# Kernel tuning notes

Measured on AMD Instinct MI355X. Metric: run time of the kernel, lower is better.

The kernel has to match this reference:

```python
import jax, jax.numpy as jnp
import numpy as np

# Architecture dims (from setArch args)
B, IN = 256, 1024          # batch, inputSize
E, H1, S = 32, 1024, 512   # numStateEnsembles, stateHiddenLayerSize, stateEnsembleOutputSize
H2, F = 512, 64            # featureHiddenLayerSize, numStateFeatures
NO, HO, OF = 16, 512, 1    # numOutputEnsembles, outputEnsembleHiddenLayerSize, outputEnsembleFeatures
T = E * F                  # thalamusSpaceSize
TIN = IN + T               # totalInputSize


def setup_inputs() -> dict:
    key = jax.random.key(0)
    ks = jax.random.split(key, 14)
    sc = 0.02
    f32 = jnp.float32
    return {
        "inputs": jax.random.normal(ks[0], (B, IN), f32),
        # stacked state-ensemble params: Linear(TIN,H1) -> Softplus -> Linear(H1,S)
        "sw1": jax.random.normal(ks[1], (E, TIN, H1), f32) * sc,
        "sb1": jax.random.normal(ks[2], (E, H1), f32) * sc,
        "sw2": jax.random.normal(ks[3], (E, H1, S), f32) * sc,
        "sb2": jax.random.normal(ks[4], (E, S), f32) * sc,
        # stacked feature-ensemble params: Linear(S,H2) -> ReLU -> Linear(H2,F)
        "fw1": jax.random.normal(ks[5], (E, S, H2), f32) * sc,
        "fb1": jax.random.normal(ks[6], (E, H2), f32) * sc,
        "fw2": jax.random.normal(ks[7], (E, H2, F), f32) * sc,
        "fb2": jax.random.normal(ks[8], (E, F), f32) * sc,
        # stacked output-ensemble params: Linear(S+1,HO) -> ReLU -> Linear(HO,OF)
        "ow1": jax.random.normal(ks[9], (NO, S + 1, HO), f32) * sc,
        "ob1": jax.random.normal(ks[10], (NO, HO), f32) * sc,
        "ow2": jax.random.normal(ks[11], (NO, HO, OF), f32) * sc,
        "ob2": jax.random.normal(ks[12], (NO, OF), f32) * sc,
        "action": 1,
        "context": 3,
        "num_iterations": 4,
    }


def reference(inputs, sw1, sb1, sw2, sb2, fw1, fb1, fw2, fb2,
              ow1, ob1, ow2, ob2, action, context, num_iterations):
    b = inputs.shape[0]
    # resetThalamus: savedThalamusFeatures = zeros(E*F)
    thal = jnp.zeros((b, T), inputs.dtype)
    state = None
    for _ in range(num_iterations):
        # leInput = cat(thalamusFeatures, inputs)  -> [B, TIN]
        x = jnp.concatenate([thal, inputs], axis=-1)
        # all E state ensembles batched: Linear -> Softplus -> Linear
        h = jax.nn.softplus(jnp.einsum('bi,eih->beh', x, sw1) + sb1)   # [B,E,H1]
        state = jnp.einsum('beh,ehs->bes', h, sw2) + sb2               # [B,E,S]
        # all E feature ensembles batched: Linear -> ReLU -> Linear
        g = jax.nn.relu(jnp.einsum('bes,esh->beh', state, fw1) + fb1)  # [B,E,H2]
        feat = jnp.einsum('beh,ehf->bef', g, fw2) + fb2                # [B,E,F]
        # thalamusFeatures = concatenate(computedFeatures)
        thal = feat.reshape(b, T)
    # output ensemble for `context` on cat([action], stateValues[context])
    sc_state = state[:, context, :]                                    # [B,S]
    a = jnp.full((b, 1), action, inputs.dtype)
    y = jnp.concatenate([a, sc_state], axis=-1)                        # [B,S+1]
    z = jax.nn.relu(y @ ow1[context] + ob1[context])                   # [B,HO]
    reward = z @ ow2[context] + ob2[context]                           # [B,OF]
    return reward
```

## Files before the change

### kernel.cpp

```cpp
#include <hip/hip_runtime.h>
#include <hip/hip_bf16.h>

#define B_SZ 256
#define IN_  1024
#define E_   32
#define H1_  1024
#define S_   512
#define H2_  512
#define F_   64
#define T_   2048
#define TIN_ 3072
#define NO_  16
#define HO_  512

typedef __attribute__((ext_vector_type(8))) short bf16x8;
typedef __attribute__((ext_vector_type(4))) float f32x4;

__device__ __forceinline__ unsigned short f2bf(float f) {
    unsigned u = __builtin_bit_cast(unsigned, f);
    u += 0x7fffu + ((u >> 16) & 1u);
    return (unsigned short)(u >> 16);
}
__device__ __forceinline__ float bf2f(unsigned short h) {
    return __builtin_bit_cast(float, ((unsigned)h) << 16);
}
__device__ __forceinline__ float softplusf(float x) {
    return fmaxf(x, 0.0f) + log1pf(expf(-fabsf(x)));
}
__device__ __forceinline__ void gload_lds16(const void* g, void* l) {
    __builtin_amdgcn_global_load_lds(
        (const __attribute__((address_space(1))) unsigned int*)g,
        (__attribute__((address_space(3))) unsigned int*)l,
        16, 0, 0);
}

__global__ __launch_bounds__(256) void cvt_t64(const float* __restrict__ in,
                                               unsigned short* __restrict__ out,
                                               int K, int N) {
    __shared__ float tile[64][65];
    const size_t eoff = (size_t)blockIdx.z * K * N;
    const float* ip = in + eoff;
    unsigned short* op = out + eoff;
    const int k0 = blockIdx.x * 64, n0 = blockIdx.y * 64;
    const int t = threadIdx.x;
    const int lr = t >> 4;
    const int lc = (t & 15) << 2;
    #pragma unroll
    for (int i = 0; i < 4; ++i) {
        const float4 v = *(const float4*)&ip[(size_t)(k0 + lr + 16 * i) * N + n0 + lc];
        float* dst = &tile[lr + 16 * i][lc];
        dst[0] = v.x; dst[1] = v.y; dst[2] = v.z; dst[3] = v.w;
    }
    __syncthreads();
    #pragma unroll
    for (int i = 0; i < 4; ++i) {
        const int n = (t >> 4) + 16 * i;
        const int k = (t & 15) << 2;
        ushort4 o;
        o.x = f2bf(tile[k][n]); o.y = f2bf(tile[k + 1][n]);
        o.z = f2bf(tile[k + 2][n]); o.w = f2bf(tile[k + 3][n]);
        *(ushort4*)&op[(size_t)(n0 + n) * K + k0 + k] = o;
    }
}

__global__ void x_init(const float* __restrict__ inp, unsigned short* __restrict__ x) {
    const int i = blockIdx.x * 256 + threadIdx.x;
    const int b = i / (IN_ / 4), c = (i % (IN_ / 4)) * 4;
    const float4 v = *(const float4*)&inp[(size_t)b * IN_ + c];
    ushort4 o;
    o.x = f2bf(v.x); o.y = f2bf(v.y); o.z = f2bf(v.z); o.w = f2bf(v.w);
    *(ushort4*)&x[(size_t)b * TIN_ + T_ + c] = o;
}

template<int BM, int BN, int TPB, int ACT, int ADD_BASE, int OUTM>
__global__ __launch_bounds__(TPB) void gemm_k(
    const unsigned short* __restrict__ A, int lda, long strideAe,
    int kOff, int K,
    const unsigned short* __restrict__ W, int ldw, long strideWe,
    const float* __restrict__ bias,
    const float* __restrict__ baseBuf,
    void* __restrict__ out, void* __restrict__ out2,
    int ldc, long strideOe, int N)
{
    constexpr int NW = TPB / 64;
    constexpr int WM_ = 2, WN_ = NW / 2;
    constexpr int MI = BM / (16 * WM_), NI = BN / (16 * WN_);
    constexpr int AL = (BM * 4) / TPB, BL = (BN * 4) / TPB;
    __shared__ unsigned short As0[BM * 32], Bs0[BN * 32];
    __shared__ unsigned short As1[BM * 32], Bs1[BN * 32];
    const int e = blockIdx.z;
    const int m0 = blockIdx.x * BM;
    const int n0 = blockIdx.y * BN;
    const int tid = threadIdx.x;
    const int wid = tid >> 6;
    const int lane = tid & 63;
    const int wm = wid / WN_, wn = wid % WN_;
    const unsigned short* Ae = A + (size_t)e * strideAe + (size_t)m0 * lda + kOff;
    const unsigned short* We = W + (size_t)e * strideWe + (size_t)n0 * ldw + kOff;

    f32x4 acc[MI][NI];
    #pragma unroll
    for (int i = 0; i < MI; ++i)
        #pragma unroll
        for (int j = 0; j < NI; ++j) {
            f32x4 z = {0.f, 0.f, 0.f, 0.f};
            acc[i][j] = z;
        }

    const int lr = lane & 15;
    const int lk = (lane >> 4) << 3;

    auto stage = [&](unsigned short* Asb, unsigned short* Bsb, int kt) {
        const int kk = kt * 32;
        #pragma unroll
        for (int p = 0; p < AL; ++p) {
            const int seg = p * TPB + tid;
            const int r = seg >> 2, c = (seg & 3) << 3;
            gload_lds16(Ae + (size_t)r * lda + kk + c, Asb + ((size_t)(p * TPB + wid * 64)) * 8);
        }
        #pragma unroll
        for (int p = 0; p < BL; ++p) {
            const int seg = p * TPB + tid;
            const int r = seg >> 2, c = (seg & 3) << 3;
            gload_lds16(We + (size_t)r * ldw + kk + c, Bsb + ((size_t)(p * TPB + wid * 64)) * 8);
        }
    };
    auto compute = [&](const unsigned short* Asb, const unsigned short* Bsb) {
        bf16x8 af[MI], bfv[NI];
        #pragma unroll
        for (int mi = 0; mi < MI; ++mi)
            af[mi] = *(const bf16x8*)&Asb[(wm * MI * 16 + mi * 16 + lr) * 32 + lk];
        #pragma unroll
        for (int ni = 0; ni < NI; ++ni)
            bfv[ni] = *(const bf16x8*)&Bsb[(wn * NI * 16 + ni * 16 + lr) * 32 + lk];
        #pragma unroll
        for (int mi = 0; mi < MI; ++mi)
            #pragma unroll
            for (int ni = 0; ni < NI; ++ni)
                acc[mi][ni] = __builtin_amdgcn_mfma_f32_16x16x32_bf16(
                    af[mi], bfv[ni], acc[mi][ni], 0, 0, 0);
    };

    const int nt = K / 32;
    stage(As0, Bs0, 0);
    __syncthreads();
    for (int t = 0; t < nt; t += 2) {
        stage(As1, Bs1, t + 1);
        compute(As0, Bs0);
        __syncthreads();
        if (t + 2 < nt) stage(As0, Bs0, t + 2);
        compute(As1, Bs1);
        __syncthreads();
    }

    const int lg = lane >> 4;
    #pragma unroll
    for (int ni = 0; ni < NI; ++ni) {
        const int col = n0 + wn * NI * 16 + ni * 16 + lr;
        const float bv = bias ? bias[(size_t)e * N + col] : 0.0f;
        #pragma unroll
        for (int mi = 0; mi < MI; ++mi) {
            #pragma unroll
            for (int r = 0; r < 4; ++r) {
                const int row = m0 + wm * MI * 16 + mi * 16 + lg * 4 + r;
                float v = acc[mi][ni][r] + bv;
                if constexpr (ADD_BASE) v += baseBuf[((size_t)e * B_SZ + row) * H1_ + col];
                if constexpr (ACT == 1) v = softplusf(v);
                if constexpr (ACT == 2) v = fmaxf(v, 0.0f);
                const size_t oidx = (size_t)e * strideOe + (size_t)row * ldc + col;
                if constexpr (OUTM == 2) {
                    ((float*)out)[oidx] = v;
                    ((unsigned short*)out2)[oidx] = f2bf(softplusf(v));
                } else {
                    ((unsigned short*)out)[oidx] = f2bf(v);
                }
            }
        }
    }
}

__global__ __launch_bounds__(512) void head_z(const unsigned short* __restrict__ state,
                                              const float* __restrict__ ow1,
                                              const float* __restrict__ ob1,
                                              const int* __restrict__ actp,
                                              const int* __restrict__ ctxp,
                                              float* __restrict__ z) {
    __shared__ float ys[16][516];
    const int ctx = *ctxp;
    const float act = (float)(*actp);
    const int b0 = blockIdx.x * 16;
    const int t = threadIdx.x;
    for (int bb = 0; bb < 16; ++bb)
        ys[bb][1 + t] = bf2f(state[((size_t)(ctx * B_SZ + b0 + bb)) * S_ + t]);
    if (t < 16) ys[t][0] = act;
    __syncthreads();
    const float* w = ow1 + (size_t)ctx * (S_ + 1) * HO_;
    float acc[16];
    #pragma unroll
    for (int bb = 0; bb < 16; ++bb) acc[bb] = 0.0f;
    for (int k = 0; k < S_ + 1; ++k) {
        const float wv = w[(size_t)k * HO_ + t];
        #pragma unroll
        for (int bb = 0; bb < 16; ++bb) acc[bb] += ys[bb][k] * wv;
    }
    const float b1 = ob1[ctx * HO_ + t];
    for (int bb = 0; bb < 16; ++bb)
        z[(size_t)(b0 + bb) * HO_ + t] = fmaxf(acc[bb] + b1, 0.0f);
}

__global__ void head_r(const float* __restrict__ z, const float* __restrict__ ow2,
                       const float* __restrict__ ob2, const int* __restrict__ ctxp,
                       float* __restrict__ out) {
    const int ctx = *ctxp;
    const int b = blockIdx.x;
    const int t = threadIdx.x;
    const float* w = ow2 + (size_t)ctx * HO_;
    float s = 0.0f;
    for (int h = t; h < HO_; h += 64) s += z[(size_t)b * HO_ + h] * w[h];
    #pragma unroll
    for (int off = 32; off; off >>= 1) s += __shfl_down(s, off);
    if (t == 0) out[b] = s + ob2[ctx];
}

extern "C" void kernel_launch(void* const* d_in, const int* in_sizes, int n_in,
                              void* d_out, int out_size, void* d_ws, size_t ws_size,
                              hipStream_t stream) {
    (void)in_sizes; (void)n_in; (void)out_size; (void)ws_size;
    const float* inputs = (const float*)d_in[0];
    const float* sw1 = (const float*)d_in[1];
    const float* sb1 = (const float*)d_in[2];
    const float* sw2 = (const float*)d_in[3];
    const float* sb2 = (const float*)d_in[4];
    const float* fw1 = (const float*)d_in[5];
    const float* fb1 = (const float*)d_in[6];
    const float* fw2 = (const float*)d_in[7];
    const float* fb2 = (const float*)d_in[8];
    const float* ow1 = (const float*)d_in[9];
    const float* ob1 = (const float*)d_in[10];
    const float* ow2 = (const float*)d_in[11];
    const float* ob2 = (const float*)d_in[12];
    const int* actp = (const int*)d_in[13];
    const int* ctxp = (const int*)d_in[14];

    char* p = (char*)d_ws;
    unsigned short* w1t = (unsigned short*)p; p += (size_t)E_ * H1_ * TIN_ * 2;
    unsigned short* w2t = (unsigned short*)p; p += (size_t)E_ * S_ * H1_ * 2;
    unsigned short* f1t = (unsigned short*)p; p += (size_t)E_ * H2_ * S_ * 2;
    unsigned short* f2t = (unsigned short*)p; p += (size_t)E_ * F_ * H2_ * 2;
    unsigned short* xbf = (unsigned short*)p; p += (size_t)B_SZ * TIN_ * 2;
    float* base = (float*)p;                  p += (size_t)E_ * B_SZ * H1_ * 4;
    unsigned short* hbf = (unsigned short*)p; p += (size_t)E_ * B_SZ * H1_ * 2;
    unsigned short* stbf = (unsigned short*)p; p += (size_t)E_ * B_SZ * S_ * 2;
    unsigned short* gbf = (unsigned short*)p; p += (size_t)E_ * B_SZ * H2_ * 2;
    float* zbuf = (float*)p;                  p += (size_t)B_SZ * HO_ * 4;

    cvt_t64<<<dim3(TIN_ / 64, H1_ / 64, E_), 256, 0, stream>>>(sw1, w1t, TIN_, H1_);
    cvt_t64<<<dim3(H1_ / 64, S_ / 64, E_),  256, 0, stream>>>(sw2, w2t, H1_, S_);
    cvt_t64<<<dim3(S_ / 64, H2_ / 64, E_),  256, 0, stream>>>(fw1, f1t, S_, H2_);
    cvt_t64<<<dim3(H2_ / 64, F_ / 64, E_),  256, 0, stream>>>(fw2, f2t, H2_, F_);
    x_init<<<(B_SZ * IN_ / 4) / 256, 256, 0, stream>>>(inputs, xbf);

    gemm_k<128, 128, 512, 0, 0, 2><<<dim3(2, H1_ / 128, E_), 512, 0, stream>>>(
        xbf, TIN_, 0L, T_, IN_, w1t, TIN_, (long)H1_ * TIN_, sb1, nullptr,
        base, hbf, H1_, (long)B_SZ * H1_, H1_);

    for (int it = 0; it < 4; ++it) {
        if (it > 0) {
            gemm_k<128, 128, 512, 1, 1, 0><<<dim3(2, H1_ / 128, E_), 512, 0, stream>>>(
                xbf, TIN_, 0L, 0, T_, w1t, TIN_, (long)H1_ * TIN_, nullptr, base,
                hbf, nullptr, H1_, (long)B_SZ * H1_, H1_);
        }
        gemm_k<64, 64, 256, 0, 0, 0><<<dim3(4, S_ / 64, E_), 256, 0, stream>>>(
            hbf, H1_, (long)B_SZ * H1_, 0, H1_, w2t, H1_, (long)S_ * H1_, sb2, nullptr,
            stbf, nullptr, S_, (long)B_SZ * S_, S_);
        if (it < 3) {
            gemm_k<64, 64, 256, 2, 0, 0><<<dim3(4, H2_ / 64, E_), 256, 0, stream>>>(
                stbf, S_, (long)B_SZ * S_, 0, S_, f1t, S_, (long)H2_ * S_, fb1, nullptr,
                gbf, nullptr, H2_, (long)B_SZ * H2_, H2_);
            gemm_k<64, 64, 256, 0, 0, 0><<<dim3(4, 1, E_), 256, 0, stream>>>(
                gbf, H2_, (long)B_SZ * H2_, 0, H2_, f2t, H2_, (long)F_ * H2_, fb2, nullptr,
                xbf, nullptr, TIN_, 64L, F_);
        }
    }
    head_z<<<B_SZ / 16, 512, 0, stream>>>(stbf, ow1, ob1, actp, ctxp, zbuf);
    head_r<<<B_SZ, 64, 0, stream>>>(zbuf, ow2, ob2, ctxp, (float*)d_out);
}
```

Before: 804.2 us.

## Add swizzled 64-wide-K GEMM kernel with interleaved MFMA/LDS scheduling for main layers

```diff
diff --git a/kernel.cpp b/kernel.cpp
--- a/kernel.cpp
+++ b/kernel.cpp
@@ -70,6 +70,171 @@
     ushort4 o;
     o.x = f2bf(v.x); o.y = f2bf(v.y); o.z = f2bf(v.z); o.w = f2bf(v.w);
     *(ushort4*)&x[(size_t)b * TIN_ + T_ + c] = o;
+}
+
+#define RD_A(RHALF, PTR)                                                          \
+    _Pragma("unroll") for (int i_ = 0; i_ < 2; ++i_)                              \
+    _Pragma("unroll") for (int kh_ = 0; kh_ < 2; ++kh_) {                         \
+        const int mi_ = (RHALF) * 2 + i_;                                         \
+        const int row_ = wm * 64 + mi_ * 16 + lr;                                 \
+        af[mi_][kh_] = *(const bf16x8*)((PTR) + row_ * 64 +                       \
+                       ((((kh_ << 2) + lg) ^ (row_ & 7)) << 3));                  \
+    }
+#define RD_B(NHALF, PTR)                                                          \
+    _Pragma("unroll") for (int j_ = 0; j_ < 2; ++j_)                              \
+    _Pragma("unroll") for (int kh_ = 0; kh_ < 2; ++kh_) {                         \
+        const int ni_ = (NHALF) * 2 + j_;                                         \
+        const int row_ = wn * 64 + ni_ * 16 + lr;                                 \
+        bfr[ni_][kh_] = *(const bf16x8*)((PTR) + row_ * 64 +                      \
+                        ((((kh_ << 2) + lg) ^ (row_ & 7)) << 3));                 \
+    }
+#define MMQ(RH, NH)                                                               \
+    _Pragma("unroll") for (int i_ = 0; i_ < 2; ++i_)                              \
+    _Pragma("unroll") for (int j_ = 0; j_ < 2; ++j_)                              \
+    _Pragma("unroll") for (int kh_ = 0; kh_ < 2; ++kh_)                           \
+        acc[(RH)*2+i_][(NH)*2+j_] = __builtin_amdgcn_mfma_f32_16x16x32_bf16(      \
+            af[(RH)*2+i_][kh_], bfr[(NH)*2+j_][kh_], acc[(RH)*2+i_][(NH)*2+j_],   \
+            0, 0, 0);
+
+template<int TPB, int ACT, int ADD_BASE, int OUTM>
+__global__ __launch_bounds__(TPB, 2) void gemm8(
+    const unsigned short* __restrict__ A, int lda, long strideAe,
+    int kOff, int K,
+    const unsigned short* __restrict__ W, int ldw, long strideWe,
+    const float* __restrict__ bias,
+    const float* __restrict__ baseBuf,
+    void* __restrict__ out, void* __restrict__ out2,
+    int ldc, long strideOe, int N)
+{
+    constexpr int BM = 128;
+    constexpr int NW = TPB / 64;
+    constexpr int WN_ = NW / 2;
+    constexpr int BN = 64 * WN_;
+    constexpr int RA = (64 * 8) / TPB;
+    constexpr int RB = ((BN / 2) * 8) / TPB;
+    constexpr int LQ = 2 * (RA + RB);
+
+    __shared__ unsigned short As[2][BM * 64];
+    __shared__ unsigned short Bs[2][BN * 64];
+
+    const int NB = N / BN;
+    const int bid = blockIdx.x;
+    const int pairs = gridDim.x >> 1;
+    const int mhalf = (bid >= pairs) ? 1 : 0;
+    const int pr = bid - mhalf * pairs;
+    const int n0 = (pr % NB) * BN;
+    const int e  = pr / NB;
+    const int m0 = mhalf * BM;
+
+    const int tid = threadIdx.x;
+    const int wid = tid >> 6;
+    const int lane = tid & 63;
+    const int wm = wid / WN_, wn = wid % WN_;
+    const int lr = lane & 15;
+    const int lg = lane >> 4;
+
+    const unsigned short* Ae = A + (size_t)e * strideAe + (size_t)m0 * lda + kOff;
+    const unsigned short* We = W + (size_t)e * strideWe + (size_t)n0 * ldw + kOff;
+
+    f32x4 acc[4][4];
+    #pragma unroll
+    for (int i = 0; i < 4; ++i)
+        #pragma unroll
+        for (int j = 0; j < 4; ++j) {
+            f32x4 z = {0.f, 0.f, 0.f, 0.f};
+            acc[i][j] = z;
+        }
+    bf16x8 af[4][2], bfr[4][2];
+
+    auto issueGroup = [&](int kt, int bufI) {
+        const int kk = kt << 6;
+        unsigned short* Ad = &As[bufI][0];
+        unsigned short* Bd = &Bs[bufI][0];
+        #pragma unroll
+        for (int h = 0; h < 2; ++h)
+            #pragma unroll
+            for (int rr = 0; rr < RA; ++rr) {
+                const int seg = rr * TPB + tid;
+                const int row = h * 64 + (seg >> 3);
+                gload_lds16(Ae + (size_t)row * lda + kk + (((seg & 7) ^ (row & 7)) << 3),
+                            Ad + (size_t)(h * 64 * 64) + (size_t)(rr * TPB + (wid << 6)) * 8);
+            }
+        #pragma unroll
+        for (int h = 0; h < 2; ++h)
+            #pragma unroll
+            for (int rr = 0; rr < RB; ++rr) {
+                const int seg = rr * TPB + tid;
+                const int row = h * (BN / 2) + (seg >> 3);
+                gload_lds16(We + (size_t)row * ldw + kk + (((seg & 7) ^ (row & 7)) << 3),
+                            Bd + (size_t)(h * (BN / 2) * 64) + (size_t)(rr * TPB + (wid << 6)) * 8);
+            }
+    };
+
+    const int nt = K >> 6;
+    issueGroup(0, 0);
+    if (nt > 1) issueGroup(1, 1);
+
+    for (int t = 0; t < nt; ++t) {
+        const int c = t & 1;
+        const unsigned short* Ab = &As[c][0];
+        const unsigned short* Bb = &Bs[c][0];
+        if (t + 1 < nt) { asm volatile("s_waitcnt vmcnt(%0)" :: "i"(LQ) : "memory"); }
+        else            { asm volatile("s_waitcnt vmcnt(0)" ::: "memory"); }
+        __builtin_amdgcn_sched_barrier(0);
+        __builtin_amdgcn_s_barrier();
+        RD_A(0, Ab); RD_B(0, Bb);
+        asm volatile("s_waitcnt lgkmcnt(0)" ::: "memory");
+        __builtin_amdgcn_sched_barrier(0);
+        __builtin_amdgcn_s_setprio(1);
+        MMQ(0, 0);
+        __builtin_amdgcn_s_setprio(0);
+        __builtin_amdgcn_s_barrier();
+        RD_B(1, Bb);
+        asm volatile("s_waitcnt lgkmcnt(0)" ::: "memory");
+        __builtin_amdgcn_sched_barrier(0);
+        __builtin_amdgcn_s_setprio(1);
+        MMQ(0, 1);
+        __builtin_amdgcn_s_setprio(0);
+        __builtin_amdgcn_s_barrier();
+        RD_A(1, Ab);
+        asm volatile("s_waitcnt lgkmcnt(0)" ::: "memory");
+        __builtin_amdgcn_sched_barrier(0);
+        __builtin_amdgcn_s_setprio(1);
+        MMQ(1, 0);
+        __builtin_amdgcn_s_setprio(0);
+        __builtin_amdgcn_s_barrier();
+        __builtin_amdgcn_sched_barrier(0);
+        if (t + 2 < nt) issueGroup(t + 2, c);
+        __builtin_amdgcn_sched_barrier(0);
+        __builtin_amdgcn_s_setprio(1);
+        MMQ(1, 1);
+        __builtin_amdgcn_s_setprio(0);
+    }
+
+    #pragma unroll
+    for (int ni = 0; ni < 4; ++ni) {
+        const int col = n0 + wn * 64 + ni * 16 + lr;
+        const float bv = bias ? bias[(size_t)e * N + col] : 0.0f;
+        #pragma unroll
+        for (int mi = 0; mi < 4; ++mi) {
+            #pragma unroll
+            for (int r = 0; r < 4; ++r) {
+                const int row = m0 + wm * 64 + mi * 16 + lg * 4 + r;
+                float v = acc[mi][ni][r] + bv;
+                if constexpr (ADD_BASE) v += baseBuf[((size_t)e * B_SZ + row) * H1_ + col];
+                if constexpr (ACT == 1) v = softplusf(v);
+                if constexpr (ACT == 2) v = fmaxf(v, 0.0f);
+                const size_t oidx = (size_t)e * strideOe + (size_t)row * ldc + col;
+                if constexpr (OUTM == 2) {
+                    ((float*)out)[oidx] = v;
+                    ((unsigned short*)out2)[oidx] = f2bf(softplusf(v));
+                } else {
+                    ((unsigned short*)out)[oidx] = f2bf(v);
+                }
+            }
+        }
+    }
+    (void)out2;
 }
 
 template<int BM, int BN, int TPB, int ACT, int ADD_BASE, int OUTM>
@@ -106,7 +271,6 @@
             f32x4 z = {0.f, 0.f, 0.f, 0.f};
             acc[i][j] = z;
         }
-
     const int lr = lane & 15;
     const int lk = (lane >> 4) << 3;
 
@@ -126,10 +290,10 @@
         }
     };
     auto compute = [&](const unsigned short* Asb, const unsigned short* Bsb) {
-        bf16x8 af[MI], bfv[NI];
+        bf16x8 af2[MI], bfv[NI];
         #pragma unroll
         for (int mi = 0; mi < MI; ++mi)
-            af[mi] = *(const bf16x8*)&Asb[(wm * MI * 16 + mi * 16 + lr) * 32 + lk];
+            af2[mi] = *(const bf16x8*)&Asb[(wm * MI * 16 + mi * 16 + lr) * 32 + lk];
         #pragma unroll
         for (int ni = 0; ni < NI; ++ni)
             bfv[ni] = *(const bf16x8*)&Bsb[(wn * NI * 16 + ni * 16 + lr) * 32 + lk];
@@ -138,7 +302,7 @@
             #pragma unroll
             for (int ni = 0; ni < NI; ++ni)
                 acc[mi][ni] = __builtin_amdgcn_mfma_f32_16x16x32_bf16(
-                    af[mi], bfv[ni], acc[mi][ni], 0, 0, 0);
+                    af2[mi], bfv[ni], acc[mi][ni], 0, 0, 0);
     };
 
     const int nt = K / 32;
@@ -177,6 +341,7 @@
             }
         }
     }
+    (void)out2;
 }
 
 __global__ __launch_bounds__(512) void head_z(const unsigned short* __restrict__ state,
@@ -260,21 +425,21 @@
     cvt_t64<<<dim3(H2_ / 64, F_ / 64, E_),  256, 0, stream>>>(fw2, f2t, H2_, F_);
     x_init<<<(B_SZ * IN_ / 4) / 256, 256, 0, stream>>>(inputs, xbf);
 
-    gemm_k<128, 128, 512, 0, 0, 2><<<dim3(2, H1_ / 128, E_), 512, 0, stream>>>(
+    gemm8<512, 0, 0, 2><<<dim3(2 * 4 * E_), 512, 0, stream>>>(
         xbf, TIN_, 0L, T_, IN_, w1t, TIN_, (long)H1_ * TIN_, sb1, nullptr,
         base, hbf, H1_, (long)B_SZ * H1_, H1_);
 
     for (int it = 0; it < 4; ++it) {
         if (it > 0) {
-            gemm_k<128, 128, 512, 1, 1, 0><<<dim3(2, H1_ / 128, E_), 512, 0, stream>>>(
+            gemm8<512, 1, 1, 0><<<dim3(2 * 4 * E_), 512, 0, stream>>>(
                 xbf, TIN_, 0L, 0, T_, w1t, TIN_, (long)H1_ * TIN_, nullptr, base,
                 hbf, nullptr, H1_, (long)B_SZ * H1_, H1_);
         }
-        gemm_k<64, 64, 256, 0, 0, 0><<<dim3(4, S_ / 64, E_), 256, 0, stream>>>(
+        gemm8<256, 0, 0, 0><<<dim3(2 * 4 * E_), 256, 0, stream>>>(
             hbf, H1_, (long)B_SZ * H1_, 0, H1_, w2t, H1_, (long)S_ * H1_, sb2, nullptr,
             stbf, nullptr, S_, (long)B_SZ * S_, S_);
         if (it < 3) {
-            gemm_k<64, 64, 256, 2, 0, 0><<<dim3(4, H2_ / 64, E_), 256, 0, stream>>>(
+            gemm8<256, 2, 0, 0><<<dim3(2 * 4 * E_), 256, 0, stream>>>(
                 stbf, S_, (long)B_SZ * S_, 0, S_, f1t, S_, (long)H2_ * S_, fb1, nullptr,
                 gbf, nullptr, H2_, (long)B_SZ * H2_, H2_);
             gemm_k<64, 64, 256, 0, 0, 0><<<dim3(4, 1, E_), 256, 0, stream>>>(
```

After: 931.4 us. 15.8% more time.

## Add full-batch GEMM kernel with triple-buffered LDS pipeline and XOR swizzle

Applied to the files above, without the earlier changes.

```diff
diff --git a/kernel.cpp b/kernel.cpp
--- a/kernel.cpp
+++ b/kernel.cpp
@@ -70,6 +70,143 @@
     ushort4 o;
     o.x = f2bf(v.x); o.y = f2bf(v.y); o.z = f2bf(v.z); o.w = f2bf(v.w);
     *(ushort4*)&x[(size_t)b * TIN_ + T_ + c] = o;
+}
+
+template<int BN, int WM, int WN, int ACT, int ADD_BASE, int OUTM>
+__global__ __launch_bounds__(512, 2) void gemmr(
+    const unsigned short* __restrict__ A, int lda, long strideAe,
+    int kOff, int K,
+    const unsigned short* __restrict__ W, int ldw, long strideWe,
+    const float* __restrict__ bias,
+    const float* __restrict__ baseBuf,
+    void* __restrict__ out, void* __restrict__ out2,
+    int ldc, long strideOe, int N)
+{
+    constexpr int BM = 256;
+    constexpr int TPB = 512;
+    constexpr int MI = BM / (16 * WM);
+    constexpr int NI = BN / (16 * WN);
+    constexpr int RA = BM * 8 / TPB;
+    constexpr int RB = BN * 8 / TPB;
+    constexpr int L  = RA + RB;
+
+    __shared__ unsigned short As[3][BM * 64];
+    __shared__ unsigned short Bs[3][BN * 64];
+
+    const int NB = N / BN;
+    const int bid = blockIdx.x;
+    const int n0 = (bid % NB) * BN;
+    const int e  = bid / NB;
+
+    const int tid = threadIdx.x;
+    const int wid = tid >> 6;
+    const int lane = tid & 63;
+    const int wm = wid / WN, wn = wid % WN;
+    const int lr = lane & 15;
+    const int lg = lane >> 4;
+
+    const unsigned short* Ae = A + (size_t)e * strideAe + kOff;
+    const unsigned short* We = W + (size_t)e * strideWe + (size_t)n0 * ldw + kOff;
+
+    f32x4 acc[MI][NI];
+    #pragma unroll
+    for (int i = 0; i < MI; ++i)
+        #pragma unroll
+        for (int j = 0; j < NI; ++j) {
+            f32x4 z = {0.f, 0.f, 0.f, 0.f};
+            acc[i][j] = z;
+        }
+
+    auto issueGroup = [&](int kt, int bufI) {
+        const int kk = kt << 6;
+        unsigned short* Ad = &As[bufI][0];
+        unsigned short* Bd = &Bs[bufI][0];
+        #pragma unroll
+        for (int rr = 0; rr < RA; ++rr) {
+            const int seg = rr * TPB + tid;
+            const int row = seg >> 3;
+            gload_lds16(Ae + (size_t)row * lda + kk + (((seg & 7) ^ (row & 7)) << 3),
+                        Ad + (size_t)(rr * TPB + (wid << 6)) * 8);
+        }
+        #pragma unroll
+        for (int rr = 0; rr < RB; ++rr) {
+            const int seg = rr * TPB + tid;
+            const int row = seg >> 3;
+            gload_lds16(We + (size_t)row * ldw + kk + (((seg & 7) ^ (row & 7)) << 3),
+                        Bd + (size_t)(rr * TPB + (wid << 6)) * 8);
+        }
+    };
+
+    const int nt = K >> 6;
+    issueGroup(0, 0);
+    issueGroup(1, 1);
+    issueGroup(2, 2);
+
+    int c = 0;
+    for (int u = 0; u < nt; ++u) {
+        const unsigned short* Ab = &As[c][0];
+        const unsigned short* Bb = &Bs[c][0];
+        if (u + 2 < nt)      { asm volatile("s_waitcnt vmcnt(%0)" :: "i"(2 * L) : "memory"); }
+        else if (u + 1 < nt) { asm volatile("s_waitcnt vmcnt(%0)" :: "i"(L) : "memory"); }
+        else                 { asm volatile("s_waitcnt vmcnt(0)" ::: "memory"); }
+        __builtin_amdgcn_s_barrier();
+        __builtin_amdgcn_sched_barrier(0);
+
+        bf16x8 af[MI][2], bfr[NI][2];
+        #pragma unroll
+        for (int mi = 0; mi < MI; ++mi)
+            #pragma unroll
+            for (int kh = 0; kh < 2; ++kh) {
+                const int row = wm * (MI * 16) + mi * 16 + lr;
+                af[mi][kh] = *(const bf16x8*)(Ab + row * 64 + ((((kh << 2) + lg) ^ (row & 7)) << 3));
+            }
+        #pragma unroll
+        for (int ni = 0; ni < NI; ++ni)
+            #pragma unroll
+            for (int kh = 0; kh < 2; ++kh) {
+                const int row = wn * (NI * 16) + ni * 16 + lr;
+                bfr[ni][kh] = *(const bf16x8*)(Bb + row * 64 + ((((kh << 2) + lg) ^ (row & 7)) << 3));
+            }
+        #pragma unroll
+        for (int mi = 0; mi < MI; ++mi)
+            #pragma unroll
+            for (int ni = 0; ni < NI; ++ni)
+                #pragma unroll
+                for (int kh = 0; kh < 2; ++kh)
+                    acc[mi][ni] = __builtin_amdgcn_mfma_f32_16x16x32_bf16(
+                        af[mi][kh], bfr[ni][kh], acc[mi][ni], 0, 0, 0);
+
+        asm volatile("s_waitcnt lgkmcnt(0)" ::: "memory");
+        __builtin_amdgcn_s_barrier();
+        __builtin_amdgcn_sched_barrier(0);
+        if (u + 3 < nt) issueGroup(u + 3, c);
+        c = (c == 2) ? 0 : c + 1;
+    }
+
+    #pragma unroll
+    for (int ni = 0; ni < NI; ++ni) {
+        const int col = n0 + wn * (NI * 16) + ni * 16 + lr;
+        const float bv = bias ? bias[(size_t)e * N + col] : 0.0f;
+        #pragma unroll
+        for (int mi = 0; mi < MI; ++mi) {
+            #pragma unroll
+            for (int r = 0; r < 4; ++r) {
+                const int row = wm * (MI * 16) + mi * 16 + lg * 4 + r;
+                float v = acc[mi][ni][r] + bv;
+                if constexpr (ADD_BASE) v += baseBuf[((size_t)e * B_SZ + row) * H1_ + col];
+                if constexpr (ACT == 1) v = softplusf(v);
+                if constexpr (ACT == 2) v = fmaxf(v, 0.0f);
+                const size_t oidx = (size_t)e * strideOe + (size_t)row * ldc + col;
+                if constexpr (OUTM == 2) {
+                    ((float*)out)[oidx] = v;
+                    ((unsigned short*)out2)[oidx] = f2bf(softplusf(v));
+                } else {
+                    ((unsigned short*)out)[oidx] = f2bf(v);
+                }
+            }
+        }
+    }
+    (void)out2;
 }
 
 template<int BM, int BN, int TPB, int ACT, int ADD_BASE, int OUTM>
@@ -106,7 +243,6 @@
             f32x4 z = {0.f, 0.f, 0.f, 0.f};
             acc[i][j] = z;
         }
-
     const int lr = lane & 15;
     const int lk = (lane >> 4) << 3;
 
@@ -115,21 +251,21 @@
         #pragma unroll
         for (int p = 0; p < AL; ++p) {
             const int seg = p * TPB + tid;
-            const int r = seg >> 2, c = (seg & 3) << 3;
-            gload_lds16(Ae + (size_t)r * lda + kk + c, Asb + ((size_t)(p * TPB + wid * 64)) * 8);
+            const int r = seg >> 2, cc = (seg & 3) << 3;
+            gload_lds16(Ae + (size_t)r * lda + kk + cc, Asb + ((size_t)(p * TPB + wid * 64)) * 8);
         }
         #pragma unroll
         for (int p = 0; p < BL; ++p) {
             const int seg = p * TPB + tid;
-            const int r = seg >> 2, c = (seg & 3) << 3;
-            gload_lds16(We + (size_t)r * ldw + kk + c, Bsb + ((size_t)(p * TPB + wid * 64)) * 8);
+            const int r = seg >> 2, cc = (seg & 3) << 3;
+            gload_lds16(We + (size_t)r * ldw + kk + cc, Bsb + ((size_t)(p * TPB + wid * 64)) * 8);
         }
     };
     auto compute = [&](const unsigned short* Asb, const unsigned short* Bsb) {
-        bf16x8 af[MI], bfv[NI];
+        bf16x8 af2[MI], bfv[NI];
         #pragma unroll
         for (int mi = 0; mi < MI; ++mi)
-            af[mi] = *(const bf16x8*)&Asb[(wm * MI * 16 + mi * 16 + lr) * 32 + lk];
+            af2[mi] = *(const bf16x8*)&Asb[(wm * MI * 16 + mi * 16 + lr) * 32 + lk];
         #pragma unroll
         for (int ni = 0; ni < NI; ++ni)
             bfv[ni] = *(const bf16x8*)&Bsb[(wn * NI * 16 + ni * 16 + lr) * 32 + lk];
@@ -138,7 +274,7 @@
             #pragma unroll
             for (int ni = 0; ni < NI; ++ni)
                 acc[mi][ni] = __builtin_amdgcn_mfma_f32_16x16x32_bf16(
-                    af[mi], bfv[ni], acc[mi][ni], 0, 0, 0);
+                    af2[mi], bfv[ni], acc[mi][ni], 0, 0, 0);
     };
 
     const int nt = K / 32;
@@ -177,6 +313,7 @@
             }
         }
     }
+    (void)out2;
 }
 
 __global__ __launch_bounds__(512) void head_z(const unsigned short* __restrict__ state,
@@ -260,21 +397,21 @@
     cvt_t64<<<dim3(H2_ / 64, F_ / 64, E_),  256, 0, stream>>>(fw2, f2t, H2_, F_);
     x_init<<<(B_SZ * IN_ / 4) / 256, 256, 0, stream>>>(inputs, xbf);
 
-    gemm_k<128, 128, 512, 0, 0, 2><<<dim3(2, H1_ / 128, E_), 512, 0, stream>>>(
+    gemmr<128, 4, 2, 0, 0, 2><<<dim3((H1_ / 128) * E_), 512, 0, stream>>>(
         xbf, TIN_, 0L, T_, IN_, w1t, TIN_, (long)H1_ * TIN_, sb1, nullptr,
         base, hbf, H1_, (long)B_SZ * H1_, H1_);
 
     for (int it = 0; it < 4; ++it) {
         if (it > 0) {
-            gemm_k<128, 128, 512, 1, 1, 0><<<dim3(2, H1_ / 128, E_), 512, 0, stream>>>(
+            gemmr<128, 4, 2, 1, 1, 0><<<dim3((H1_ / 128) * E_), 512, 0, stream>>>(
                 xbf, TIN_, 0L, 0, T_, w1t, TIN_, (long)H1_ * TIN_, nullptr, base,
                 hbf, nullptr, H1_, (long)B_SZ * H1_, H1_);
         }
-        gemm_k<64, 64, 256, 0, 0, 0><<<dim3(4, S_ / 64, E_), 256, 0, stream>>>(
+        gemmr<64, 8, 1, 0, 0, 0><<<dim3((S_ / 64) * E_), 512, 0, stream>>>(
             hbf, H1_, (long)B_SZ * H1_, 0, H1_, w2t, H1_, (long)S_ * H1_, sb2, nullptr,
             stbf, nullptr, S_, (long)B_SZ * S_, S_);
         if (it < 3) {
-            gemm_k<64, 64, 256, 2, 0, 0><<<dim3(4, H2_ / 64, E_), 256, 0, stream>>>(
+            gemmr<64, 8, 1, 2, 0, 0><<<dim3((H2_ / 64) * E_), 512, 0, stream>>>(
                 stbf, S_, (long)B_SZ * S_, 0, S_, f1t, S_, (long)H2_ * S_, fb1, nullptr,
                 gbf, nullptr, H2_, (long)B_SZ * H2_, H2_);
             gemm_k<64, 64, 256, 0, 0, 0><<<dim3(4, 1, E_), 256, 0, stream>>>(
```

Result: slower. 947.7 us (+17.8%).
